# Optimization experiments

Measured on AMD Instinct MI355X. Metric: run time of the kernel, lower is better.

The kernel has to match this reference:

```python
import jax, jax.numpy as jnp
import numpy as np

N = 100000
E = 400000
NFEAT, NHID, NOUT, NHEAD = 128, 64, 128, 4
HIDDEN = NHID * NHEAD  # 256
SLOPE = 0.2


def gat_conv(x, src, dst, W, a_src, a_dst, b, concat):
    """PyG-style GATConv (eval mode, self-loops already appended to src/dst).
    x: [N, Fin]; W: [Fin, H*C]; a_src/a_dst: [H, C]; b: [H*C] or [C]."""
    H, C = a_src.shape
    h = (x @ W).reshape(N, H, C)                      # [N,H,C]
    al_s = (h * a_src).sum(-1)                        # [N,H] per-node src score
    al_d = (h * a_dst).sum(-1)                        # [N,H] per-node dst score
    e = jax.nn.leaky_relu(al_s[src] + al_d[dst], SLOPE)  # [Et,H]
    # segment softmax over incoming edges of each dst node
    m = jax.ops.segment_max(e, dst, num_segments=N)
    m = jnp.where(jnp.isfinite(m), m, 0.0)
    ex = jnp.exp(e - m[dst])
    denom = jax.ops.segment_sum(ex, dst, num_segments=N)
    alpha = ex / (denom[dst] + 1e-16)                 # [Et,H]
    msg = alpha[:, :, None] * h[src]                  # [Et,H,C]
    out = jax.ops.segment_sum(msg, dst, num_segments=N)  # [N,H,C]
    out = out.reshape(N, H * C) if concat else out.mean(axis=1)
    return out + b


def setup_inputs() -> dict:
    key = jax.random.key(0)
    ks = jax.random.split(key, 16)
    x = jax.random.normal(ks[0], (N, NFEAT), dtype=jnp.float32)
    edge_index = jax.random.randint(ks[1], (2, E), 0, N, dtype=jnp.int64)
    s = 0.1
    inp = {
        'x': x, 'edge_index': edge_index,
        # layer 0: nfeat -> nhid x nhead (concat)
        'W0': jax.random.normal(ks[2], (NFEAT, HIDDEN), jnp.float32) * s,
        'as0': jax.random.normal(ks[3], (NHEAD, NHID), jnp.float32) * s,
        'ad0': jax.random.normal(ks[4], (NHEAD, NHID), jnp.float32) * s,
        'b0': jnp.zeros((HIDDEN,), jnp.float32),
        # layer 1: hidden -> nhid x nhead (concat)
        'W1': jax.random.normal(ks[5], (HIDDEN, HIDDEN), jnp.float32) * s,
        'as1': jax.random.normal(ks[6], (NHEAD, NHID), jnp.float32) * s,
        'ad1': jax.random.normal(ks[7], (NHEAD, NHID), jnp.float32) * s,
        'b1': jnp.zeros((HIDDEN,), jnp.float32),
        # output layer: hidden -> nout, heads=1, concat=False
        'W2': jax.random.normal(ks[8], (HIDDEN, NOUT), jnp.float32) * s,
        'as2': jax.random.normal(ks[9], (1, NOUT), jnp.float32) * s,
        'ad2': jax.random.normal(ks[10], (1, NOUT), jnp.float32) * s,
        'b2': jnp.zeros((NOUT,), jnp.float32),
    }
    return inp


def reference(x, edge_index, W0, as0, ad0, b0, W1, as1, ad1, b1, W2, as2, ad2, b2):
    # PyG GATConv adds self-loops by default; edge set is shared across layers.
    loop = jnp.arange(N, dtype=edge_index.dtype)
    src = jnp.concatenate([edge_index[0], loop])
    dst = jnp.concatenate([edge_index[1], loop])
    # dropout inactive in eval mode
    h = jax.nn.elu(gat_conv(x, src, dst, W0, as0, ad0, b0, concat=True))
    h = jax.nn.elu(gat_conv(h, src, dst, W1, as1, ad1, b1, concat=True))
    out = gat_conv(h, src, dst, W2, as2, ad2, b2, concat=False)
    return out
```

## Files before the change

### kernel.cpp

```cpp
#include <hip/hip_runtime.h>
#include <cmath>

#define NN 100000
#define EE 400000
#define ET (EE + NN)
#define SLOPE 0.2f

typedef __attribute__((ext_vector_type(8))) short short8;
typedef __attribute__((ext_vector_type(4))) float floatx4;

__device__ __forceinline__ float b2f(ushort u) {
    union { unsigned int i; float f; } v; v.i = ((unsigned int)u) << 16; return v.f;
}
__device__ __forceinline__ float bl(uint u) {
    union { unsigned int i; float f; } v; v.i = u << 16; return v.f;
}
__device__ __forceinline__ float bh(uint u) {
    union { unsigned int i; float f; } v; v.i = u & 0xffff0000u; return v.f;
}
__device__ __forceinline__ ushort f2b(float f) {
    union { float f; unsigned int i; } v; v.f = f;
    unsigned int r = v.i + 0x7FFFu + ((v.i >> 16) & 1u);
    return (ushort)(r >> 16);
}

__global__ __launch_bounds__(256) void count_deg(const int* __restrict__ ei, int* __restrict__ deg) {
    int e = blockIdx.x * 256 + threadIdx.x;
    if (e < EE) atomicAdd(&deg[ei[EE + e]], 1);
}

__global__ __launch_bounds__(256) void scan1(const int* __restrict__ deg, int* __restrict__ incl,
                                             int* __restrict__ bsums) {
    __shared__ int ts[256];
    int b = blockIdx.x, t = threadIdx.x;
    int base = b * 1024 + t * 4;
    int v[4];
#pragma unroll
    for (int i = 0; i < 4; i++) {
        int n = base + i;
        v[i] = (n < NN) ? (deg[n] + 1) : 0;
    }
    int s = 0;
#pragma unroll
    for (int i = 0; i < 4; i++) { s += v[i]; v[i] = s; }
    ts[t] = s;
    __syncthreads();
    for (int off = 1; off < 256; off <<= 1) {
        int x = (t >= off) ? ts[t - off] : 0;
        __syncthreads();
        ts[t] += x;
        __syncthreads();
    }
    int excl = ts[t] - s;
#pragma unroll
    for (int i = 0; i < 4; i++) {
        int n = base + i;
        if (n < NN) incl[n] = v[i] + excl;
    }
    if (t == 255) bsums[b] = ts[255];
}

__global__ __launch_bounds__(128) void scan2(int* __restrict__ bsums, int nblk) {
    __shared__ int ts[128];
    int t = threadIdx.x;
    int v = (t < nblk) ? bsums[t] : 0;
    ts[t] = v;
    __syncthreads();
    for (int off = 1; off < 128; off <<= 1) {
        int x = (t >= off) ? ts[t - off] : 0;
        __syncthreads();
        ts[t] += x;
        __syncthreads();
    }
    if (t < nblk) bsums[t] = ts[t] - v;
}

__global__ __launch_bounds__(256) void scan3(const int* __restrict__ incl, const int* __restrict__ deg,
                                             const int* __restrict__ bsums, int* __restrict__ row_ptr,
                                             int* __restrict__ cursor) {
    int n = blockIdx.x * 256 + threadIdx.x;
    if (n < NN) {
        int rp = incl[n] - (deg[n] + 1) + bsums[n >> 10];
        row_ptr[n] = rp;
        cursor[n] = rp;
    }
    if (n == 0) row_ptr[NN] = ET;
}

__global__ __launch_bounds__(256) void scatter(const int* __restrict__ ei, int* __restrict__ cursor,
                                               int* __restrict__ col) {
    int e = blockIdx.x * 256 + threadIdx.x;
    if (e < EE) {
        int d = ei[EE + e];
        int p = atomicAdd(&cursor[d], 1);
        col[p] = ei[e];
    }
}

__global__ __launch_bounds__(256) void selfloop(const int* __restrict__ cursor, int* __restrict__ col) {
    int n = blockIdx.x * 256 + threadIdx.x;
    if (n < NN) col[cursor[n]] = n;
}

__global__ __launch_bounds__(256) void cast_to_bf16(const float* __restrict__ in,
                                                    ushort* __restrict__ out, int n4) {
    int i = blockIdx.x * 256 + threadIdx.x;
    if (i < n4) {
        float4 v = ((const float4*)in)[i];
        ushort4 o;
        o.x = f2b(v.x); o.y = f2b(v.y); o.z = f2b(v.z); o.w = f2b(v.w);
        ((ushort4*)out)[i] = o;
    }
}

__global__ __launch_bounds__(256) void transpose_cast_all(const float* __restrict__ W0,
                                                          const float* __restrict__ W1,
                                                          const float* __restrict__ W2,
                                                          ushort* __restrict__ Wt0,
                                                          ushort* __restrict__ Wt1,
                                                          ushort* __restrict__ Wt2) {
    int idx = blockIdx.x * 256 + threadIdx.x;
    if (idx < 32768) {
        int n = idx >> 7, k = idx & 127;
        Wt0[idx] = f2b(W0[(size_t)k * 256 + n]);
    } else if (idx < 32768 + 65536) {
        int j = idx - 32768;
        int n = j >> 8, k = j & 255;
        Wt1[j] = f2b(W1[(size_t)k * 256 + n]);
    } else if (idx < 131072) {
        int j = idx - 98304;
        int n = j >> 8, k = j & 255;
        Wt2[j] = f2b(W2[(size_t)k * 128 + n]);
    }
}

#define LP 40
__global__ __launch_bounds__(256) void gemm_bf16(const ushort* __restrict__ A,
                                                 const ushort* __restrict__ Bt,
                                                 ushort* __restrict__ C,
                                                 int M, int K, int N,
                                                 const float* __restrict__ asf,
                                                 const float* __restrict__ adf,
                                                 float* __restrict__ als,
                                                 float* __restrict__ ald,
                                                 int H, int lgC) {
    __shared__ ushort As[128 * LP];
    __shared__ ushort Bs[128 * LP];
    int tid = threadIdx.x;
    int bm = blockIdx.x * 128;
    int bn = blockIdx.y * 128;
    int wave = tid >> 6, lane = tid & 63;
    int wm = (wave >> 1) * 64, wn = (wave & 1) * 64;

    floatx4 acc[4][4];
#pragma unroll
    for (int i = 0; i < 4; i++)
#pragma unroll
        for (int j = 0; j < 4; j++) acc[i][j] = (floatx4)0.f;

    int r = tid >> 1;
    int c = (tid & 1) * 16;

    int frow = lane & 15;
    int kq = (lane >> 4) * 8;

    for (int k0 = 0; k0 < K; k0 += 32) {
        uint4 a0, a1;
        if (bm + r < M) {
            const uint4* ap = (const uint4*)(A + (size_t)(bm + r) * K + k0 + c);
            a0 = ap[0]; a1 = ap[1];
        } else {
            a0 = make_uint4(0, 0, 0, 0); a1 = a0;
        }
        *(uint4*)&As[r * LP + c]     = a0;
        *(uint4*)&As[r * LP + c + 8] = a1;

        const uint4* bp = (const uint4*)(Bt + (size_t)(bn + r) * K + k0 + c);
        *(uint4*)&Bs[r * LP + c]     = bp[0];
        *(uint4*)&Bs[r * LP + c + 8] = bp[1];

        __syncthreads();

        short8 afr[4], bfr[4];
#pragma unroll
        for (int i = 0; i < 4; i++)
            afr[i] = *(const short8*)&As[(wm + i * 16 + frow) * LP + kq];
#pragma unroll
        for (int j = 0; j < 4; j++)
            bfr[j] = *(const short8*)&Bs[(wn + j * 16 + frow) * LP + kq];
#pragma unroll
        for (int i = 0; i < 4; i++)
#pragma unroll
            for (int j = 0; j < 4; j++)
                acc[i][j] = __builtin_amdgcn_mfma_f32_16x16x32_bf16(afr[i], bfr[j], acc[i][j], 0, 0, 0);

        __syncthreads();
    }

    int ccol = bn + wn + (lane & 15);
    int crow = bm + wm + (lane >> 4) * 4;
#pragma unroll
    for (int i = 0; i < 4; i++) {
#pragma unroll
        for (int reg = 0; reg < 4; reg++) {
            int row = crow + i * 16 + reg;
            if (row < M) {
#pragma unroll
                for (int j = 0; j < 4; j++)
                    C[(size_t)row * N + ccol + j * 16] = f2b(acc[i][j][reg]);
            }
        }
    }

    {
        int cb = bn + wn + (lane & 15);
        float asv[4], adv[4];
#pragma unroll
        for (int j = 0; j < 4; j++) {
            asv[j] = asf[cb + j * 16];
            adv[j] = adf[cb + j * 16];
        }
        int hidx = (bn + wn) >> lgC;
#pragma unroll
        for (int i = 0; i < 4; i++) {
#pragma unroll
            for (int reg = 0; reg < 4; reg++) {
                float ss = acc[i][0][reg] * asv[0] + acc[i][1][reg] * asv[1]
                         + acc[i][2][reg] * asv[2] + acc[i][3][reg] * asv[3];
                float dd = acc[i][0][reg] * adv[0] + acc[i][1][reg] * adv[1]
                         + acc[i][2][reg] * adv[2] + acc[i][3][reg] * adv[3];
#pragma unroll
                for (int off = 1; off < 16; off <<= 1) {
                    ss += __shfl_xor(ss, off, 64);
                    dd += __shfl_xor(dd, off, 64);
                }
                int row = crow + i * 16 + reg;
                if ((lane & 15) == 0 && row < M) {
                    if (lgC == 6) {
                        als[row * H + hidx] = ss;
                        ald[row * H + hidx] = dd;
                    } else {
                        atomicAdd(&als[row], ss);
                        atomicAdd(&ald[row], dd);
                    }
                }
            }
        }
    }
}

template <int H, int HC, bool ELU_ACT, bool OUT_BF16>
__global__ __launch_bounds__(256) void aggregate2(const ushort* __restrict__ hlin,
                                                  const float* __restrict__ als,
                                                  const float* __restrict__ ald,
                                                  const int* __restrict__ row_ptr,
                                                  const int* __restrict__ col,
                                                  const float* __restrict__ bias,
                                                  void* __restrict__ outv) {
    constexpr int CP = HC / 32;
    constexpr int GS = 32 / H;
    constexpr int NU = CP / 2;
    int wv = threadIdx.x >> 6, lane = threadIdx.x & 63;
    int hl = lane & 31;
    int dst = blockIdx.x * 8 + wv * 2 + (lane >> 5);
    int rs = row_ptr[dst];
    int deg = row_ptr[dst + 1] - rs;
    int eg = hl & (GS - 1);
    int head = hl / GS;
    float ad = ald[dst * H + head];
    uint uoff = (uint)hl * NU;

    float acc[CP];
#pragma unroll
    for (int j = 0; j < CP; j++) acc[j] = 0.f;

    int degB = __shfl_xor(deg, 32, 64);

    if (deg <= GS) {
        int src = 0;
        float s = -1e30f;
        if (eg < deg) {
            src = col[rs + eg];
            float sc = als[src * H + head] + ad;
            s = sc > 0.f ? sc : SLOPE * sc;
        }
        float m = s;
#pragma unroll
        for (int off = 1; off < GS; off <<= 1) m = fmaxf(m, __shfl_xor(m, off, 64));
        float e = (eg < deg) ? __expf(s - m) : 0.f;
        float sum = e;
#pragma unroll
        for (int off = 1; off < GS; off <<= 1) sum += __shfl_xor(sum, off, 64);
        float w = e * (1.0f / (sum + 1e-16f));

        int mdeg = max(deg, (degB <= GS) ? degB : 0);
        int sbase = lane & 32;
        int wbase = (lane & 32) | (hl & ~(GS - 1));

        for (int d = 0; d < mdeg; d += 4) {
            int s0 = __shfl(src, sbase + d, 64);
            int s1 = __shfl(src, sbase + d + 1, 64);
            int s2 = __shfl(src, sbase + d + 2, 64);
            int s3 = __shfl(src, sbase + d + 3, 64);
            float w0 = __shfl(w, wbase + d, 64);
            float w1 = __shfl(w, wbase + d + 1, 64);
            float w2 = __shfl(w, wbase + d + 2, 64);
            float w3 = __shfl(w, wbase + d + 3, 64);
            const uint* p0 = (const uint*)(hlin + (size_t)s0 * HC) + uoff;
            const uint* p1 = (const uint*)(hlin + (size_t)s1 * HC) + uoff;
            const uint* p2 = (const uint*)(hlin + (size_t)s2 * HC) + uoff;
            const uint* p3 = (const uint*)(hlin + (size_t)s3 * HC) + uoff;
            uint u0[NU], u1[NU], u2[NU], u3[NU];
#pragma unroll
            for (int q = 0; q < NU; q++) { u0[q] = p0[q]; u1[q] = p1[q]; u2[q] = p2[q]; u3[q] = p3[q]; }
#pragma unroll
            for (int q = 0; q < NU; q++) {
                acc[2*q]   += w0 * bl(u0[q]) + w1 * bl(u1[q]) + w2 * bl(u2[q]) + w3 * bl(u3[q]);
                acc[2*q+1] += w0 * bh(u0[q]) + w1 * bh(u1[q]) + w2 * bh(u2[q]) + w3 * bh(u3[q]);
            }
        }
    } else {
        float m = -1e30f;
        for (int e2 = eg; e2 < deg; e2 += GS) {
            int s0 = col[rs + e2];
            float sc = als[s0 * H + head] + ad;
            sc = sc > 0.f ? sc : SLOPE * sc;
            m = fmaxf(m, sc);
        }
#pragma unroll
        for (int off = 1; off < GS; off <<= 1) m = fmaxf(m, __shfl_xor(m, off, 64));
        float sum = 0.f;
        for (int e2 = eg; e2 < deg; e2 += GS) {
            int s0 = col[rs + e2];
            float sc = als[s0 * H + head] + ad;
            sc = sc > 0.f ? sc : SLOPE * sc;
            sum += __expf(sc - m);
        }
#pragma unroll
        for (int off = 1; off < GS; off <<= 1) sum += __shfl_xor(sum, off, 64);
        float inv = 1.0f / (sum + 1e-16f);
        for (int d = 0; d < deg; d++) {
            int sd = col[rs + d];
            float sc = als[sd * H + head] + ad;
            sc = sc > 0.f ? sc : SLOPE * sc;
            float wd = __expf(sc - m) * inv;
            const uint* p = (const uint*)(hlin + (size_t)sd * HC) + uoff;
#pragma unroll
            for (int q = 0; q < NU; q++) {
                uint u = p[q];
                acc[2*q]   += wd * bl(u);
                acc[2*q+1] += wd * bh(u);
            }
        }
    }

#pragma unroll
    for (int j = 0; j < CP; j++) {
        float v = acc[j] + bias[hl * CP + j];
        if (ELU_ACT) v = v > 0.f ? v : (__expf(v) - 1.0f);
        acc[j] = v;
    }
    if (OUT_BF16) {
        uint* outp = (uint*)((ushort*)outv + (size_t)dst * HC) + uoff;
        uint pk[NU];
#pragma unroll
        for (int q = 0; q < NU; q++)
            pk[q] = (uint)f2b(acc[2*q]) | ((uint)f2b(acc[2*q+1]) << 16);
#pragma unroll
        for (int q = 0; q < NU; q++) outp[q] = pk[q];
    } else {
        float* outp = (float*)outv + (size_t)dst * HC + hl * CP;
#pragma unroll
        for (int j = 0; j < CP; j++) outp[j] = acc[j];
    }
}

extern "C" void kernel_launch(void* const* d_in, const int* in_sizes, int n_in,
                              void* d_out, int out_size, void* d_ws, size_t ws_size,
                              hipStream_t stream) {
    const float* x   = (const float*)d_in[0];
    const int*   ei  = (const int*)d_in[1];
    const float* W0  = (const float*)d_in[2];
    const float* as0 = (const float*)d_in[3];
    const float* ad0 = (const float*)d_in[4];
    const float* b0  = (const float*)d_in[5];
    const float* W1  = (const float*)d_in[6];
    const float* as1 = (const float*)d_in[7];
    const float* ad1 = (const float*)d_in[8];
    const float* b1  = (const float*)d_in[9];
    const float* W2  = (const float*)d_in[10];
    const float* as2 = (const float*)d_in[11];
    const float* ad2 = (const float*)d_in[12];
    const float* b2  = (const float*)d_in[13];
    float* out = (float*)d_out;

    char* ws = (char*)d_ws;
    size_t off = 0;
    auto alloc = [&](size_t bytes) {
        void* p = ws + off;
        off += (bytes + 255) & ~(size_t)255;
        return p;
    };
    ushort* xb   = (ushort*)alloc((size_t)NN * 128 * 2);
    ushort* h    = (ushort*)alloc((size_t)NN * 256 * 2);
    ushort* actB = (ushort*)alloc((size_t)NN * 256 * 2);
    ushort* actC = (ushort*)alloc((size_t)NN * 256 * 2);
    ushort* Wt0  = (ushort*)alloc((size_t)256 * 128 * 2);
    ushort* Wt1  = (ushort*)alloc((size_t)256 * 256 * 2);
    ushort* Wt2  = (ushort*)alloc((size_t)128 * 256 * 2);
    float* als   = (float*)alloc((size_t)NN * 4 * 4);
    float* ald   = (float*)alloc((size_t)NN * 4 * 4);
    int* deg     = (int*)alloc((size_t)NN * 4);
    int* incl    = (int*)alloc((size_t)NN * 4);
    int* row_ptr = (int*)alloc((size_t)(NN + 1) * 4);
    int* cursor  = (int*)alloc((size_t)NN * 4);
    int* col     = (int*)alloc((size_t)ET * 4);
    int* bsums   = (int*)alloc(128 * 4);

    const int NBLK = (NN + 1023) / 1024;

    hipMemsetAsync(deg, 0, (size_t)NN * 4, stream);
    count_deg<<<(EE + 255) / 256, 256, 0, stream>>>(ei, deg);
    scan1<<<NBLK, 256, 0, stream>>>(deg, incl, bsums);
    scan2<<<1, 128, 0, stream>>>(bsums, NBLK);
    scan3<<<(NN + 255) / 256, 256, 0, stream>>>(incl, deg, bsums, row_ptr, cursor);
    scatter<<<(EE + 255) / 256, 256, 0, stream>>>(ei, cursor, col);
    selfloop<<<(NN + 255) / 256, 256, 0, stream>>>(cursor, col);

    cast_to_bf16<<<(NN * 128 / 4 + 255) / 256, 256, 0, stream>>>(x, xb, NN * 128 / 4);
    transpose_cast_all<<<(131072 + 255) / 256, 256, 0, stream>>>(W0, W1, W2, Wt0, Wt1, Wt2);

    const int GM = (NN + 127) / 128;
    const int NB8 = NN / 8;

    gemm_bf16<<<dim3(GM, 2), 256, 0, stream>>>(xb, Wt0, h, NN, 128, 256, as0, ad0, als, ald, 4, 6);
    aggregate2<4, 256, true, true><<<NB8, 256, 0, stream>>>(h, als, ald, row_ptr, col, b0, actB);

    gemm_bf16<<<dim3(GM, 2), 256, 0, stream>>>(actB, Wt1, h, NN, 256, 256, as1, ad1, als, ald, 4, 6);
    aggregate2<4, 256, true, true><<<NB8, 256, 0, stream>>>(h, als, ald, row_ptr, col, b1, actC);

    hipMemsetAsync(als, 0, (size_t)NN * 4, stream);
    hipMemsetAsync(ald, 0, (size_t)NN * 4, stream);
    gemm_bf16<<<dim3(GM, 1), 256, 0, stream>>>(actC, Wt2, h, NN, 256, 128, as2, ad2, als, ald, 1, 7);
    aggregate2<1, 128, false, false><<<NB8, 256, 0, stream>>>(h, als, ald, row_ptr, col, b2, out);
}
```

Measured before the change: 441.8 us.

## Use direct global-to-LDS loads with swizzled K=64 tiles and batch 8-edge gathers

The GEMM now stages A and B tiles through global_load_lds (bypassing registers) into an XOR-swizzled 64-wide LDS layout, and processes K in steps of 64 with two MFMA sub-steps per barrier pair. This halves the number of barriers and register round-trips. The low-degree aggregation path now gathers 8 neighbour rows per iteration with wide vector loads, raising memory-level parallelism. Activation buffers are padded so unguarded tail-row loads stay in bounds, and the layer-2 score buffers are zeroed up front.

Result: no change. 444.2 us (+0.6%).

```diff
diff --git a/kernel.cpp b/kernel.cpp
--- a/kernel.cpp
+++ b/kernel.cpp
@@ -9,9 +9,6 @@
 typedef __attribute__((ext_vector_type(8))) short short8;
 typedef __attribute__((ext_vector_type(4))) float floatx4;
 
-__device__ __forceinline__ float b2f(ushort u) {
-    union { unsigned int i; float f; } v; v.i = ((unsigned int)u) << 16; return v.f;
-}
 __device__ __forceinline__ float bl(uint u) {
     union { unsigned int i; float f; } v; v.i = u << 16; return v.f;
 }
@@ -22,6 +19,11 @@
     union { float f; unsigned int i; } v; v.f = f;
     unsigned int r = v.i + 0x7FFFu + ((v.i >> 16) & 1u);
     return (ushort)(r >> 16);
+}
+
+__device__ __forceinline__ void gload16(const ushort* g, ushort* l) {
+    __builtin_amdgcn_global_load_lds((const __attribute__((address_space(1))) void*)g,
+                                     (__attribute__((address_space(3))) void*)l, 16, 0, 0);
 }
 
 __global__ __launch_bounds__(256) void count_deg(const int* __restrict__ ei, int* __restrict__ deg) {
@@ -134,7 +136,6 @@
     }
 }
 
-#define LP 40
 __global__ __launch_bounds__(256) void gemm_bf16(const ushort* __restrict__ A,
                                                  const ushort* __restrict__ Bt,
                                                  ushort* __restrict__ C,
@@ -144,8 +145,8 @@
                                                  float* __restrict__ als,
                                                  float* __restrict__ ald,
                                                  int H, int lgC) {
-    __shared__ ushort As[128 * LP];
-    __shared__ ushort Bs[128 * LP];
+    __shared__ __attribute__((aligned(16))) ushort As[128 * 64];
+    __shared__ __attribute__((aligned(16))) ushort Bs[128 * 64];
     int tid = threadIdx.x;
     int bm = blockIdx.x * 128;
     int bn = blockIdx.y * 128;
@@ -158,42 +159,41 @@
 #pragma unroll
         for (int j = 0; j < 4; j++) acc[i][j] = (floatx4)0.f;
 
-    int r = tid >> 1;
-    int c = (tid & 1) * 16;
+    int rsub = lane >> 3;
+    int klog8 = ((lane & 7) ^ rsub) * 8;
+    const ushort* aS = A + (size_t)(bm + wave * 8 + rsub) * K + klog8;
+    const ushort* bS = Bt + (size_t)(bn + wave * 8 + rsub) * K + klog8;
+    ushort* ldsA = &As[wave * 512];
+    ushort* ldsB = &Bs[wave * 512];
 
     int frow = lane & 15;
-    int kq = (lane >> 4) * 8;
-
-    for (int k0 = 0; k0 < K; k0 += 32) {
-        uint4 a0, a1;
-        if (bm + r < M) {
-            const uint4* ap = (const uint4*)(A + (size_t)(bm + r) * K + k0 + c);
-            a0 = ap[0]; a1 = ap[1];
-        } else {
-            a0 = make_uint4(0, 0, 0, 0); a1 = a0;
-        }
-        *(uint4*)&As[r * LP + c]     = a0;
-        *(uint4*)&As[r * LP + c + 8] = a1;
-
-        const uint4* bp = (const uint4*)(Bt + (size_t)(bn + r) * K + k0 + c);
-        *(uint4*)&Bs[r * LP + c]     = bp[0];
-        *(uint4*)&Bs[r * LP + c + 8] = bp[1];
-
-        __syncthreads();
-
-        short8 afr[4], bfr[4];
-#pragma unroll
-        for (int i = 0; i < 4; i++)
-            afr[i] = *(const short8*)&As[(wm + i * 16 + frow) * LP + kq];
-#pragma unroll
-        for (int j = 0; j < 4; j++)
-            bfr[j] = *(const short8*)&Bs[(wn + j * 16 + frow) * LP + kq];
-#pragma unroll
-        for (int i = 0; i < 4; i++)
+    int q = lane >> 4;
+    int f7 = frow & 7;
+
+    for (int k0 = 0; k0 < K; k0 += 64) {
+#pragma unroll
+        for (int i = 0; i < 4; i++) {
+            gload16(aS + (size_t)i * 32 * K + k0, ldsA + i * 2048);
+            gload16(bS + (size_t)i * 32 * K + k0, ldsB + i * 2048);
+        }
+        __syncthreads();
+
+#pragma unroll
+        for (int kk = 0; kk < 2; kk++) {
+            short8 afr[4], bfr[4];
+            int phys = ((kk * 4 + q) ^ f7) * 8;
+#pragma unroll
+            for (int i = 0; i < 4; i++)
+                afr[i] = *(const short8*)&As[(wm + i * 16 + frow) * 64 + phys];
 #pragma unroll
             for (int j = 0; j < 4; j++)
-                acc[i][j] = __builtin_amdgcn_mfma_f32_16x16x32_bf16(afr[i], bfr[j], acc[i][j], 0, 0, 0);
-
+                bfr[j] = *(const short8*)&Bs[(wn + j * 16 + frow) * 64 + phys];
+#pragma unroll
+            for (int i = 0; i < 4; i++)
+#pragma unroll
+                for (int j = 0; j < 4; j++)
+                    acc[i][j] = __builtin_amdgcn_mfma_f32_16x16x32_bf16(afr[i], bfr[j], acc[i][j], 0, 0, 0);
+        }
         __syncthreads();
     }
 
@@ -245,6 +245,36 @@
                     }
                 }
             }
+        }
+    }
+}
+
+template <int NU, int HC>
+__device__ __forceinline__ void gather8(const int* sA, const float* wA,
+                                        const ushort* __restrict__ hlin, uint hl, float* acc) {
+    if constexpr (NU == 4) {
+        uint4 U[8];
+#pragma unroll
+        for (int d = 0; d < 8; d++)
+            U[d] = *((const uint4*)(hlin + (size_t)sA[d] * HC) + hl);
+#pragma unroll
+        for (int d = 0; d < 8; d++) {
+            float w = wA[d];
+            acc[0] += w * bl(U[d].x); acc[1] += w * bh(U[d].x);
+            acc[2] += w * bl(U[d].y); acc[3] += w * bh(U[d].y);
+            acc[4] += w * bl(U[d].z); acc[5] += w * bh(U[d].z);
+            acc[6] += w * bl(U[d].w); acc[7] += w * bh(U[d].w);
+        }
+    } else {
+        uint2 U[8];
+#pragma unroll
+        for (int d = 0; d < 8; d++)
+            U[d] = *((const uint2*)(hlin + (size_t)sA[d] * HC) + hl);
+#pragma unroll
+        for (int d = 0; d < 8; d++) {
+            float w = wA[d];
+            acc[0] += w * bl(U[d].x); acc[1] += w * bh(U[d].x);
+            acc[2] += w * bl(U[d].y); acc[3] += w * bh(U[d].y);
         }
     }
 }
@@ -268,7 +298,6 @@
     int eg = hl & (GS - 1);
     int head = hl / GS;
     float ad = ald[dst * H + head];
-    uint uoff = (uint)hl * NU;
 
     float acc[CP];
 #pragma unroll
@@ -293,30 +322,27 @@
         for (int off = 1; off < GS; off <<= 1) sum += __shfl_xor(sum, off, 64);
         float w = e * (1.0f / (sum + 1e-16f));
 
-        int mdeg = max(deg, (degB <= GS) ? degB : 0);
         int sbase = lane & 32;
         int wbase = (lane & 32) | (hl & ~(GS - 1));
 
-        for (int d = 0; d < mdeg; d += 4) {
-            int s0 = __shfl(src, sbase + d, 64);
-            int s1 = __shfl(src, sbase + d + 1, 64);
-            int s2 = __shfl(src, sbase + d + 2, 64);
-            int s3 = __shfl(src, sbase + d + 3, 64);
-            float w0 = __shfl(w, wbase + d, 64);
-            float w1 = __shfl(w, wbase + d + 1, 64);
-            float w2 = __shfl(w, wbase + d + 2, 64);
-            float w3 = __shfl(w, wbase + d + 3, 64);
-            const uint* p0 = (const uint*)(hlin + (size_t)s0 * HC) + uoff;
-            const uint* p1 = (const uint*)(hlin + (size_t)s1 * HC) + uoff;
-            const uint* p2 = (const uint*)(hlin + (size_t)s2 * HC) + uoff;
-            const uint* p3 = (const uint*)(hlin + (size_t)s3 * HC) + uoff;
-            uint u0[NU], u1[NU], u2[NU], u3[NU];
-#pragma unroll
-            for (int q = 0; q < NU; q++) { u0[q] = p0[q]; u1[q] = p1[q]; u2[q] = p2[q]; u3[q] = p3[q]; }
-#pragma unroll
-            for (int q = 0; q < NU; q++) {
-                acc[2*q]   += w0 * bl(u0[q]) + w1 * bl(u1[q]) + w2 * bl(u2[q]) + w3 * bl(u3[q]);
-                acc[2*q+1] += w0 * bh(u0[q]) + w1 * bh(u1[q]) + w2 * bh(u2[q]) + w3 * bh(u3[q]);
+        if constexpr (GS == 8) {
+            int sA[8]; float wA[8];
+#pragma unroll
+            for (int d = 0; d < 8; d++) {
+                sA[d] = __shfl(src, sbase + d, 64);
+                wA[d] = __shfl(w, wbase + d, 64);
+            }
+            gather8<NU, HC>(sA, wA, hlin, hl, acc);
+        } else {
+            int mdeg = max(deg, (degB <= GS) ? degB : 0);
+            for (int d0 = 0; d0 < mdeg; d0 += 8) {
+                int sA[8]; float wA[8];
+#pragma unroll
+                for (int d = 0; d < 8; d++) {
+                    sA[d] = __shfl(src, sbase + d0 + d, 64);
+                    wA[d] = __shfl(w, wbase + d0 + d, 64);
+                }
+                gather8<NU, HC>(sA, wA, hlin, hl, acc);
             }
         }
     } else {
@@ -344,12 +370,12 @@
             float sc = als[sd * H + head] + ad;
             sc = sc > 0.f ? sc : SLOPE * sc;
             float wd = __expf(sc - m) * inv;
-            const uint* p = (const uint*)(hlin + (size_t)sd * HC) + uoff;
-#pragma unroll
-            for (int q = 0; q < NU; q++) {
-                uint u = p[q];
-                acc[2*q]   += wd * bl(u);
-                acc[2*q+1] += wd * bh(u);
+            const uint* p = (const uint*)(hlin + (size_t)sd * HC) + hl * NU;
+#pragma unroll
+            for (int qq = 0; qq < NU; qq++) {
+                uint u = p[qq];
+                acc[2*qq]   += wd * bl(u);
+                acc[2*qq+1] += wd * bh(u);
             }
         }
     }
@@ -361,13 +387,13 @@
         acc[j] = v;
     }
     if (OUT_BF16) {
-        uint* outp = (uint*)((ushort*)outv + (size_t)dst * HC) + uoff;
+        uint* outp = (uint*)((ushort*)outv + (size_t)dst * HC) + hl * NU;
         uint pk[NU];
 #pragma unroll
-        for (int q = 0; q < NU; q++)
-            pk[q] = (uint)f2b(acc[2*q]) | ((uint)f2b(acc[2*q+1]) << 16);
-#pragma unroll
-        for (int q = 0; q < NU; q++) outp[q] = pk[q];
+        for (int qq = 0; qq < NU; qq++)
+            pk[qq] = (uint)f2b(acc[2*qq]) | ((uint)f2b(acc[2*qq+1]) << 16);
+#pragma unroll
+        for (int qq = 0; qq < NU; qq++) outp[qq] = pk[qq];
     } else {
         float* outp = (float*)outv + (size_t)dst * HC + hl * CP;
 #pragma unroll
@@ -401,15 +427,17 @@
         off += (bytes + 255) & ~(size_t)255;
         return p;
     };
-    ushort* xb   = (ushort*)alloc((size_t)NN * 128 * 2);
+    ushort* xb   = (ushort*)alloc((size_t)(NN + 128) * 128 * 2);
     ushort* h    = (ushort*)alloc((size_t)NN * 256 * 2);
-    ushort* actB = (ushort*)alloc((size_t)NN * 256 * 2);
-    ushort* actC = (ushort*)alloc((size_t)NN * 256 * 2);
+    ushort* actB = (ushort*)alloc((size_t)(NN + 128) * 256 * 2);
+    ushort* actC = (ushort*)alloc((size_t)(NN + 128) * 256 * 2);
     ushort* Wt0  = (ushort*)alloc((size_t)256 * 128 * 2);
     ushort* Wt1  = (ushort*)alloc((size_t)256 * 256 * 2);
     ushort* Wt2  = (ushort*)alloc((size_t)128 * 256 * 2);
     float* als   = (float*)alloc((size_t)NN * 4 * 4);
     float* ald   = (float*)alloc((size_t)NN * 4 * 4);
+    float* als2  = (float*)alloc((size_t)NN * 4);
+    float* ald2  = (float*)alloc((size_t)NN * 4);
     int* deg     = (int*)alloc((size_t)NN * 4);
     int* incl    = (int*)alloc((size_t)NN * 4);
     int* row_ptr = (int*)alloc((size_t)(NN + 1) * 4);
@@ -420,6 +448,8 @@
     const int NBLK = (NN + 1023) / 1024;
 
     hipMemsetAsync(deg, 0, (size_t)NN * 4, stream);
+    hipMemsetAsync(als2, 0, (size_t)NN * 4, stream);
+    hipMemsetAsync(ald2, 0, (size_t)NN * 4, stream);
     count_deg<<<(EE + 255) / 256, 256, 0, stream>>>(ei, deg);
     scan1<<<NBLK, 256, 0, stream>>>(deg, incl, bsums);
     scan2<<<1, 128, 0, stream>>>(bsums, NBLK);
@@ -439,8 +469,6 @@
     gemm_bf16<<<dim3(GM, 2), 256, 0, stream>>>(actB, Wt1, h, NN, 256, 256, as1, ad1, als, ald, 4, 6);
     aggregate2<4, 256, true, true><<<NB8, 256, 0, stream>>>(h, als, ald, row_ptr, col, b1, actC);
 
-    hipMemsetAsync(als, 0, (size_t)NN * 4, stream);
-    hipMemsetAsync(ald, 0, (size_t)NN * 4, stream);
-    gemm_bf16<<<dim3(GM, 1), 256, 0, stream>>>(actC, Wt2, h, NN, 256, 128, as2, ad2, als, ald, 1, 7);
-    aggregate2<1, 128, false, false><<<NB8, 256, 0, stream>>>(h, als, ald, row_ptr, col, b2, out);
-}
+    gemm_bf16<<<dim3(GM, 1), 256, 0, stream>>>(actC, Wt2, h, NN, 256, 128, as2, ad2, als2, ald2, 1, 7);
+    aggregate2<1, 128, false, false><<<NB8, 256, 0, stream>>>(h, als2, ald2, row_ptr, col, b2, out);
+}
```
